# Performance work log

Hardware: AMD Instinct MI355X
Metric: run time of the kernel (lower is better)

The kernel has to match this reference:

```python
import jax, jax.numpy as jnp
import numpy as np

IOU_THR = 0.5
SCORE_THR = 0.5
MAX_OUT = 300  # max_output_boxes_per_batch


def setup_inputs() -> dict:
    key = jax.random.key(0)
    kb, ks = jax.random.split(key)
    B, N, C = 8, 1024, 32
    u = jax.random.uniform(kb, (B, N, 4), dtype=jnp.float32)
    ctr = u[..., :2] * 100.0          # box centers in [0,100)
    sz = u[..., 2:] * 20.0 + 1.0      # box sizes in [1,21)
    # y1x1y2x2 format (as the torch module expects)
    boxes = jnp.concatenate([ctr - 0.5 * sz, ctr + 0.5 * sz], axis=-1)
    scores = jax.random.uniform(ks, (B, N, C), dtype=jnp.float32)
    return {"boxes": boxes, "scores": scores}


def _pairwise_iou(b):
    # b: [C, N, 4] in y1x1y2x2; IoU is invariant to the axis swap so no
    # conversion to x1y1x2y2 is needed.
    y1, x1, y2, x2 = b[..., 0], b[..., 1], b[..., 2], b[..., 3]
    area = (y2 - y1) * (x2 - x1)                          # [C, N]
    yy1 = jnp.maximum(y1[..., :, None], y1[..., None, :])
    xx1 = jnp.maximum(x1[..., :, None], x1[..., None, :])
    yy2 = jnp.minimum(y2[..., :, None], y2[..., None, :])
    xx2 = jnp.minimum(x2[..., :, None], x2[..., None, :])
    inter = jnp.clip(yy2 - yy1, 0.0) * jnp.clip(xx2 - xx1, 0.0)
    return inter / (area[..., :, None] + area[..., None, :] - inter)


def _nms_keep(iou, valid, thr):
    # Sequential greedy suppression, vectorized across classes.
    # iou: [C, N, N] (score-descending order), valid: [C, N] bool.
    N = iou.shape[-1]
    idx = jnp.arange(N)

    def body(i, keep):
        sup = (iou[:, i, :] > thr) & keep[:, i][:, None] & (idx[None, :] > i)
        return keep & ~sup

    return jax.lax.fori_loop(0, N, body, valid)


def _nms_single(boxes, scores):
    # boxes: [N, 4], scores: [N, C]  ->  ([M,4], [M], [M])
    N, C = scores.shape
    M = MAX_OUT
    sc = scores.T                                  # [C, N]
    valid = sc > SCORE_THR
    s = jnp.where(valid, sc, -jnp.inf)
    order = jnp.argsort(-s, axis=1, stable=True)   # per-class score desc
    sb = boxes[order]                              # [C, N, 4]
    ss = jnp.take_along_axis(s, order, axis=1)     # [C, N]
    sv = jnp.take_along_axis(valid, order, axis=1)
    keep = _nms_keep(_pairwise_iou(sb), sv, IOU_THR)   # [C, N]

    # flatten class-major (matches torch scores.transpose(1,0).flatten())
    fb = sb.reshape(C * N, 4)
    fs = ss.reshape(-1)
    fk = keep.reshape(-1)
    fcls = jnp.repeat(jnp.arange(C, dtype=jnp.int32), N)
    fbind = order.reshape(-1)                      # original box index

    # global score-descending order over kept detections, truncate to M
    g = jnp.where(fk, fs, -jnp.inf)
    gord = jnp.argsort(-g, stable=True)[:M]
    tb, ts, tc, ti, tv = fb[gord], fs[gord], fcls[gord], fbind[gord], fk[gord]

    # dedup by original box index: keep highest-score (first) occurrence;
    # torch's _get_unique_first_indices re-orders by ascending box index.
    p = jnp.arange(M, dtype=jnp.int32)
    first = jnp.full((N,), M, dtype=jnp.int32).at[ti].min(jnp.where(tv, p, M))
    present = first < M                            # [N]
    ordN = jnp.argsort(~present, stable=True)[:M]  # present box ids, ascending
    pos = first[ordN]
    m = present[ordN]
    posc = jnp.where(m, pos, 0)
    out_boxes = jnp.where(m[:, None], tb[posc], 0.0)
    out_scores = jnp.where(m, ts[posc], 0.0)
    out_classes = jnp.where(m, tc[posc], 0)
    return out_boxes, out_scores, out_classes


def reference(boxes, scores):
    ob, osc, ocl = jax.vmap(_nms_single)(boxes, scores)
    # matches torch return (output_boxes, output_scores, output_classes)
    return ob, osc, ocl
```

## Files before the change

kernel.cpp:

```cpp
#include <hip/hip_runtime.h>

#pragma clang fp contract(off)

#define NBOX   1024
#define NCLS   32
#define NBATCH 8
#define MAXOUT 300
#define SMAX   11
#define MAGIC  0x600DF00Du

#define IOU_SUP(ab, aa, bj, arj, act, acc) do {               \
    float yy1 = fmaxf((ab).x, (bj).x);                        \
    float xx1 = fmaxf((ab).y, (bj).y);                        \
    float yy2 = fminf((ab).z, (bj).z);                        \
    float xx2 = fminf((ab).w, (bj).w);                        \
    float ih = fmaxf(yy2 - yy1, 0.0f);                        \
    float iw = fmaxf(xx2 - xx1, 0.0f);                        \
    float inter = ih * iw;                                    \
    float denom = ((aa) + (arj)) - inter;                     \
    float lhs = (inter + inter) - denom;                      \
    float rhs = denom * 5.9604644775390625e-08f;              \
    if ((act) && (lhs > rhs)) (acc) |= bit;                   \
  } while (0)

__device__ __forceinline__ unsigned long long shflx64(unsigned long long v, int m) {
  unsigned lo = (unsigned)__shfl_xor((int)(unsigned)v, m, 64);
  unsigned hi = (unsigned)__shfl_xor((int)(unsigned)(v >> 32), m, 64);
  return ((unsigned long long)hi << 32) | lo;
}

__device__ __forceinline__ unsigned long long cexch(
    unsigned long long mine, int jj, int kk, int t) {
  unsigned long long other = shflx64(mine, jj);
  bool iLow = ((t & jj) == 0);
  bool desc = ((t & kk) == 0);
  bool wantMax = (iLow == desc);
  bool otherBigger = (other > mine);
  return (wantMax == otherBigger) ? other : mine;
}

__global__ __launch_bounds__(1024) void nms_fused(
    const float* __restrict__ boxes, const float* __restrict__ scores,
    unsigned long long* __restrict__ recs, unsigned int* __restrict__ flags,
    float* __restrict__ out) {
#pragma clang fp contract(off)
  const int bc = blockIdx.x;
  const int b = bc & (NBATCH - 1);
  const int c = bc >> 3;
  const int t = threadIdx.x;
  const int lane = t & 63, wav = t >> 6;

  __shared__ __align__(16) unsigned char shraw[63488];
  unsigned long long* key = (unsigned long long*)shraw;
  float4* sbox            = (float4*)(shraw + 8192);
  float* sarea            = (float*)(shraw + 24576);
  unsigned long long* mask = (unsigned long long*)(shraw + 28672);
  __shared__ unsigned long long kb[16];
  __shared__ int shV;

  const float* sp = scores + (size_t)b * NBOX * NCLS + c;
  float s = sp[(size_t)t * NCLS];
  bool valid = (s > 0.5f);
  unsigned long long mine = valid
      ? ((((unsigned long long)__float_as_uint(s)) << 32) | (unsigned)(NBOX - 1 - t))
      : (unsigned long long)(unsigned)(NBOX - 1 - t);
  if (t == 0) shV = 0;
  if (t < 16) kb[t] = 0ull;
  __syncthreads();
  unsigned long long vb = __ballot(valid);
  if (lane == 0) atomicAdd(&shV, (int)__popcll(vb));

  for (int kk = 2; kk <= 64; kk <<= 1)
    for (int jj = kk >> 1; jj > 0; jj >>= 1)
      mine = cexch(mine, jj, kk, t);
  key[t] = mine;
  __syncthreads();
  for (int kk = 128; kk <= 1024; kk <<= 1) {
    for (int jj = kk >> 1; jj >= 64; jj >>= 1) {
      if (t < 512) {
        int i = ((t & ~(jj - 1)) << 1) | (t & (jj - 1));
        int ixj = i | jj;
        unsigned long long a = key[i], bb = key[ixj];
        if (((i & kk) == 0) ? (a < bb) : (a > bb)) { key[i] = bb; key[ixj] = a; }
      }
      __syncthreads();
    }
    mine = key[t];
    for (int jj = 32; jj > 0; jj >>= 1) mine = cexch(mine, jj, kk, t);
    key[t] = mine;
    __syncthreads();
  }

  int n0 = NBOX - 1 - (int)(mine & (NBOX - 1));
  const float4* gb = (const float4*)boxes + (size_t)b * NBOX;
  float4 bx4 = gb[n0];
  sbox[t] = bx4;
  sarea[t] = (bx4.z - bx4.x) * (bx4.w - bx4.y);
  __syncthreads();
  const int V = shV;
  const int S = (V + 63) >> 6;
  const bool aj = (t < V);

  unsigned long long mext[15];
  unsigned long long mself = 0ull;
#pragma unroll
  for (int w = 0; w < 15; ++w) mext[w] = 0ull;

  if (S <= SMAX) {
    int NC = 0;
    for (int I2 = 0; I2 < S; ++I2) NC += (S - I2 + 2) / 3;
    for (int k = wav; k < NC; k += 16) {
      int I = 0, rem = k;
      for (;;) { int cI = (S - I + 2) / 3; if (rem < cI) break; rem -= cI; ++I; }
      const int J0 = I + 3 * rem;
      const bool h1 = (J0 + 1 < S), h2 = (J0 + 2 < S);
      const int j0 = (J0 << 6) + lane;
      const int j1 = h1 ? j0 + 64 : j0;
      const int j2 = h2 ? j0 + 128 : j0;
      const float4 b0 = sbox[j0]; const float ar0 = sarea[j0];
      const float4 b1 = sbox[j1]; const float ar1 = sarea[j1];
      const float4 b2 = sbox[j2]; const float ar2 = sarea[j2];
      const bool act0 = (j0 < V);
      const bool act1 = h1 && (j0 + 64 < V);
      const bool act2 = h2 && (j0 + 128 < V);
      const float4* bi = &sbox[I << 6];
      const float* ai = &sarea[I << 6];
      unsigned long long a0 = 0, a1 = 0, a2 = 0;
      unsigned long long bit = 1ull;
#pragma unroll 8
      for (int q = 0; q < 64; ++q) {
        float4 ab = bi[q];
        float aa = ai[q];
        IOU_SUP(ab, aa, b0, ar0, act0, a0);
        IOU_SUP(ab, aa, b1, ar1, act1, a1);
        IOU_SUP(ab, aa, b2, ar2, act2, a2);
        bit <<= 1;
      }
      if (rem == 0) a0 &= (1ull << lane) - 1ull;
      const int vrem = V - (I << 6);
      if (vrem < 64) {
        unsigned long long tm = (1ull << vrem) - 1ull;
        a0 &= tm; a1 &= tm; a2 &= tm;
      }
      mask[(((J0 * (J0 + 1) / 2) << 6) + lane * (J0 + 1)) + I] = a0;
      if (h1) mask[((((J0 + 1) * (J0 + 2) / 2) << 6) + lane * (J0 + 2)) + I] = a1;
      if (h2) mask[((((J0 + 2) * (J0 + 3) / 2) << 6) + lane * (J0 + 3)) + I] = a2;
    }
    __syncthreads();
    if (t < (S << 6)) {
      const int J = wav;
      const int rbs = ((J * (J + 1) / 2) << 6) + lane * (J + 1);
#pragma unroll
      for (int I = 0; I < 15; ++I)
        if (I < J) mext[I] = mask[rbs + I];
      mself = mask[rbs + J];
    }
  } else {
    const int J = wav;
    const float4 bj = sbox[t];
    const float arj = sarea[t];
#pragma unroll
    for (int I = 0; I < 16; ++I) {
      if (I <= J && (I << 6) < V) {
        unsigned long long acc = 0, bit = 1ull;
        for (int q = 0; q < 64; ++q) {
          int i = (I << 6) + q;
          float4 ab = sbox[i];
          float aa = sarea[i];
          bool act = aj && (i < t) && (i < V);
          IOU_SUP(ab, aa, bj, arj, act, acc);
          bit <<= 1;
        }
        if (I == J) mself = acc;
        else mext[I] = acc;
      }
    }
  }
  __syncthreads();

  for (int w = 0; w < S; ++w) {
    if (wav == w) {
      bool supExt = false;
#pragma unroll
      for (int i = 0; i < 15; ++i)
        if (i < w) supExt = supExt || ((mext[i] & kb[i]) != 0ull);
      bool alive = aj && !supExt;
      unsigned long long cur = __ballot(alive);
      for (;;) {
        unsigned long long nb = __ballot(alive && ((mself & cur) == 0ull));
        if (nb == cur) break;
        cur = nb;
      }
      if (lane == 0) kb[w] = cur;
    }
    __syncthreads();
  }

  unsigned long long kbr[16];
#pragma unroll
  for (int w = 0; w < 16; ++w) kbr[w] = kb[w];
  int tot = 0;
#pragma unroll
  for (int w = 0; w < 16; ++w) tot += (int)__popcll(kbr[w]);
  const size_t rbase = ((size_t)b * NCLS + c) * MAXOUT;
  unsigned long long kw = kbr[0];
#pragma unroll
  for (int w = 1; w < 16; ++w) if (w == wav) kw = kbr[w];
  if (aj && ((kw >> lane) & 1ull)) {
    int rank = 0;
#pragma unroll
    for (int w = 0; w < 16; ++w)
      if (w < wav) rank += (int)__popcll(kbr[w]);
    rank += (int)__popcll(kw & ((1ull << lane) - 1ull));
    if (rank < MAXOUT) {
      unsigned sbits = (unsigned)(mine >> 32);
      int n = NBOX - 1 - (int)(mine & (NBOX - 1));
      int flat = c * NBOX + t;
      recs[rbase + rank] = (((unsigned long long)sbits) << 32)
          | ((unsigned)(NCLS * NBOX - 1 - flat) << 10) | (unsigned)n;
    }
  }
  if (t < MAXOUT && t >= tot) recs[rbase + t] = 0ull;

  __syncthreads();
  if (t == 0)
    __hip_atomic_store(&flags[bc], MAGIC, __ATOMIC_RELEASE,
                       __HIP_MEMORY_SCOPE_AGENT);
  if (c != 0) return;

  if (t < NCLS)
    while (__hip_atomic_load(&flags[(t << 3) + b], __ATOMIC_ACQUIRE,
                             __HIP_MEMORY_SCOPE_AGENT) != MAGIC)
      __builtin_amdgcn_s_sleep(8);
  __syncthreads();

  int* histw              = (int*)shraw;
  int* hist               = (int*)(shraw + 16384);
  int* suf                = (int*)(shraw + 17408);
  unsigned long long* maxKey = (unsigned long long*)(shraw + 18448);
  unsigned long long* blist  = (unsigned long long*)(shraw + 26640);
  __shared__ int bcnt;
  __shared__ unsigned long long shT;
  __shared__ int shBstar;
  __shared__ int wcnt[16], woff[16];
  __shared__ int shPresTot;

  const int CAND = NCLS * MAXOUT;
  unsigned long long* rb = recs + (size_t)b * NCLS * MAXOUT;
  unsigned long long cand[10];
#pragma unroll
  for (int q = 0; q < 10; ++q) {
    int j = t + (q << 10);
    cand[q] = (j < CAND)
        ? __hip_atomic_load(&rb[j], __ATOMIC_RELAXED, __HIP_MEMORY_SCOPE_AGENT)
        : 0ull;
  }
  maxKey[t] = 0;
#pragma unroll
  for (int q = 0; q < 4; ++q) histw[t + (q << 10)] = 0;
  if (t == 0) { bcnt = 0; shT = 0; shBstar = -1; }
  __syncthreads();

#pragma unroll
  for (int q = 0; q < 10; ++q) {
    unsigned long long v = cand[q];
    if (v != 0ull) {
      int bk = (int)(((unsigned)(v >> 32) - 0x3F000000u) >> 15);
      atomicAdd(&histw[(wav << 8) + bk], 1);
    }
  }
  __syncthreads();
  if (t < 256) {
    int ssum = 0;
#pragma unroll
    for (int w = 0; w < 16; ++w) ssum += histw[(w << 8) + t];
    hist[t] = ssum;
  }
  __syncthreads();

  if (wav == 0) {
    int h[4];
#pragma unroll
    for (int g = 0; g < 4; ++g) h[g] = hist[g * 64 + lane];
#pragma unroll
    for (int g = 0; g < 4; ++g) {
      int v = h[g];
#pragma unroll
      for (int off = 1; off < 64; off <<= 1) {
        int u = __shfl_down(v, off);
        if (lane + off < 64) v += u;
      }
      h[g] = v;
    }
    int sum1 = __shfl(h[1], 0);
    int sum2 = __shfl(h[2], 0);
    int sum3 = __shfl(h[3], 0);
    suf[0 * 64 + lane] = h[0] + sum1 + sum2 + sum3;
    suf[1 * 64 + lane] = h[1] + sum2 + sum3;
    suf[2 * 64 + lane] = h[2] + sum3;
    suf[3 * 64 + lane] = h[3];
    if (lane == 0) suf[256] = 0;
  }
  __syncthreads();

  if (t < 256) {
    if (suf[t] >= MAXOUT && suf[t + 1] < MAXOUT) shBstar = t;
  }
  __syncthreads();
  const int Bstar = shBstar;

  if (Bstar >= 0) {
#pragma unroll
    for (int q = 0; q < 10; ++q) {
      unsigned long long v = cand[q];
      if (v != 0ull) {
        int bk = (int)(((unsigned)(v >> 32) - 0x3F000000u) >> 15);
        if (bk == Bstar) { int idx = atomicAdd(&bcnt, 1); blist[idx] = v; }
      }
    }
    __syncthreads();
    int M = bcnt;
    int need = MAXOUT - suf[Bstar + 1];
    if (t < M) {
      unsigned long long mk = blist[t];
      int r = 0;
      for (int i = 0; i < M; ++i) r += (blist[i] > mk) ? 1 : 0;
      if (r == need - 1) shT = mk;
    }
    __syncthreads();
  }
  const unsigned long long T = shT;

#pragma unroll
  for (int q = 0; q < 10; ++q) {
    unsigned long long v = cand[q];
    if (v != 0ull && v >= T) {
      int n = (int)(v & (NBOX - 1));
      atomicMax(&maxKey[n], v);
    }
  }
  __syncthreads();

  bool pres = (maxKey[t] != 0ull);
  unsigned long long wm = __ballot(pres);
  if (lane == 0) wcnt[wav] = (int)__popcll(wm);
  __syncthreads();
  if (t < 16) {
    int v = wcnt[t];
    int inc = v;
#pragma unroll
    for (int off = 1; off < 16; off <<= 1) {
      int u = __shfl_up(inc, off);
      if (lane >= off) inc += u;
    }
    woff[t] = inc - v;
    if (t == 15) shPresTot = inc;
  }
  __syncthreads();
  const int total = shPresTot;

  float* ob = out + (size_t)b * MAXOUT * 4;
  float* os = out + (size_t)NBATCH * MAXOUT * 4 + (size_t)b * MAXOUT;
  float* oc = out + (size_t)NBATCH * MAXOUT * 5 + (size_t)b * MAXOUT;

  if (pres) {
    int slot = woff[wav] + (int)__popcll(wm & ((1ull << lane) - 1ull));
    unsigned long long v = maxKey[t];
    float score = __uint_as_float((unsigned)(v >> 32));
    int flat = NCLS * NBOX - 1 - (int)((v >> 10) & (unsigned)(NCLS * NBOX - 1));
    int cls = flat >> 10;
    float4 bx = ((const float4*)boxes)[(size_t)b * NBOX + t];
    ob[slot * 4 + 0] = bx.x;
    ob[slot * 4 + 1] = bx.y;
    ob[slot * 4 + 2] = bx.z;
    ob[slot * 4 + 3] = bx.w;
    os[slot] = score;
    oc[slot] = (float)cls;
  }
  if (t >= total && t < MAXOUT) {
    ob[t * 4 + 0] = 0.0f; ob[t * 4 + 1] = 0.0f;
    ob[t * 4 + 2] = 0.0f; ob[t * 4 + 3] = 0.0f;
    os[t] = 0.0f;
    oc[t] = 0.0f;
  }
}

extern "C" void kernel_launch(void* const* d_in, const int* in_sizes, int n_in,
                              void* d_out, int out_size, void* d_ws, size_t ws_size,
                              hipStream_t stream) {
  const float* boxes  = (const float*)d_in[0];
  const float* scores = (const float*)d_in[1];
  float* out = (float*)d_out;

  unsigned long long* recs = (unsigned long long*)d_ws;
  unsigned int* flags = (unsigned int*)((char*)d_ws +
      (size_t)NBATCH * NCLS * MAXOUT * sizeof(unsigned long long));

  nms_fused<<<NBATCH * NCLS, 1024, 0, stream>>>(boxes, scores, recs, flags, out);
}
```

Baseline: 102.6 us.

## Replace IoU mask matrix with sequential greedy NMS against kept list

The full 1024-key bitonic sort is replaced by bucketing valid scores into 16 score buckets of 64, each sorted with a wave-local bitonic sort and concatenated by prefix offsets. The full-sort path stays as a fallback when a bucket overflows. The triangular pairwise IoU bitmask and its ballot fixed-point resolution are replaced by a per-wave greedy pass. Each candidate is tested only against the boxes already kept, held in shared memory, and intra-wave suppression uses readlane broadcasts of the current leader. This avoids computing IoUs for suppressed pairs and shrinks shared memory, but the work becomes serial across waves and depends on how many boxes are kept.

```diff
diff --git a/kernel.cpp b/kernel.cpp
--- a/kernel.cpp
+++ b/kernel.cpp
@@ -6,22 +6,22 @@
 #define NCLS   32
 #define NBATCH 8
 #define MAXOUT 300
-#define SMAX   11
 #define MAGIC  0x600DF00Du
 
-#define IOU_SUP(ab, aa, bj, arj, act, acc) do {               \
-    float yy1 = fmaxf((ab).x, (bj).x);                        \
-    float xx1 = fmaxf((ab).y, (bj).y);                        \
-    float yy2 = fminf((ab).z, (bj).z);                        \
-    float xx2 = fminf((ab).w, (bj).w);                        \
-    float ih = fmaxf(yy2 - yy1, 0.0f);                        \
-    float iw = fmaxf(xx2 - xx1, 0.0f);                        \
-    float inter = ih * iw;                                    \
-    float denom = ((aa) + (arj)) - inter;                     \
-    float lhs = (inter + inter) - denom;                      \
-    float rhs = denom * 5.9604644775390625e-08f;              \
-    if ((act) && (lhs > rhs)) (acc) |= bit;                   \
-  } while (0)
+__device__ __forceinline__ bool sup_pred(float4 a, float aa, float4 bj, float arj) {
+#pragma clang fp contract(off)
+  float yy1 = fmaxf(a.x, bj.x);
+  float xx1 = fmaxf(a.y, bj.y);
+  float yy2 = fminf(a.z, bj.z);
+  float xx2 = fminf(a.w, bj.w);
+  float ih = fmaxf(yy2 - yy1, 0.0f);
+  float iw = fmaxf(xx2 - xx1, 0.0f);
+  float inter = ih * iw;
+  float denom = (aa + arj) - inter;
+  float lhs = (inter + inter) - denom;
+  float rhs = denom * 5.9604644775390625e-08f;
+  return lhs > rhs;
+}
 
 __device__ __forceinline__ unsigned long long shflx64(unsigned long long v, int m) {
   unsigned lo = (unsigned)__shfl_xor((int)(unsigned)v, m, 64);
@@ -37,6 +37,10 @@
   bool wantMax = (iLow == desc);
   bool otherBigger = (other > mine);
   return (wantMax == otherBigger) ? other : mine;
+}
+
+__device__ __forceinline__ float bcastf(float v, int p) {
+  return __uint_as_float((unsigned)__builtin_amdgcn_readlane((int)__float_as_uint(v), p));
 }
 
 __global__ __launch_bounds__(1024) void nms_fused(
@@ -50,13 +54,13 @@
   const int t = threadIdx.x;
   const int lane = t & 63, wav = t >> 6;
 
-  __shared__ __align__(16) unsigned char shraw[63488];
-  unsigned long long* key = (unsigned long long*)shraw;
-  float4* sbox            = (float4*)(shraw + 8192);
-  float* sarea            = (float*)(shraw + 24576);
-  unsigned long long* mask = (unsigned long long*)(shraw + 28672);
-  __shared__ unsigned long long kb[16];
-  __shared__ int shV;
+  __shared__ __align__(16) unsigned char shraw[36864];
+  unsigned long long* skey   = (unsigned long long*)shraw;
+  unsigned long long* bstage = (unsigned long long*)(shraw + 8192);
+  float4* kbox               = (float4*)(shraw + 16384);
+  float* karea               = (float*)(shraw + 32768);
+  __shared__ int bcount[16];
+  __shared__ int shOVF, shK;
 
   const float* sp = scores + (size_t)b * NBOX * NCLS + c;
   float s = sp[(size_t)t * NCLS];
@@ -64,162 +68,114 @@
   unsigned long long mine = valid
       ? ((((unsigned long long)__float_as_uint(s)) << 32) | (unsigned)(NBOX - 1 - t))
       : (unsigned long long)(unsigned)(NBOX - 1 - t);
-  if (t == 0) shV = 0;
-  if (t < 16) kb[t] = 0ull;
-  __syncthreads();
-  unsigned long long vb = __ballot(valid);
-  if (lane == 0) atomicAdd(&shV, (int)__popcll(vb));
-
-  for (int kk = 2; kk <= 64; kk <<= 1)
-    for (int jj = kk >> 1; jj > 0; jj >>= 1)
-      mine = cexch(mine, jj, kk, t);
-  key[t] = mine;
-  __syncthreads();
-  for (int kk = 128; kk <= 1024; kk <<= 1) {
-    for (int jj = kk >> 1; jj >= 64; jj >>= 1) {
-      if (t < 512) {
-        int i = ((t & ~(jj - 1)) << 1) | (t & (jj - 1));
-        int ixj = i | jj;
-        unsigned long long a = key[i], bb = key[ixj];
-        if (((i & kk) == 0) ? (a < bb) : (a > bb)) { key[i] = bb; key[ixj] = a; }
-      }
+  if (t < 16) bcount[t] = 0;
+  if (t == 0) { shOVF = 0; shK = 0; }
+  __syncthreads();
+
+  if (valid) {
+    int sbk = 15 - (int)((__float_as_uint(s) - 0x3F000000u) >> 19);
+    int slot = atomicAdd(&bcount[sbk], 1);
+    if (slot < 64) bstage[(sbk << 6) + slot] = mine;
+    else shOVF = 1;
+  }
+  __syncthreads();
+
+  int cval = (lane < 16) ? bcount[lane] : 0;
+  int incl = cval;
+#pragma unroll
+  for (int o = 1; o < 16; o <<= 1) {
+    int u = __shfl_up(incl, o);
+    if (lane >= o) incl += u;
+  }
+  const int V = __builtin_amdgcn_readlane(incl, 15);
+  const int myoff = __builtin_amdgcn_readlane(incl, wav) - bcount[wav];
+  const int mycnt = bcount[wav];
+
+  if (!shOVF) {
+    unsigned long long kreg = (lane < mycnt) ? bstage[(wav << 6) + lane] : 0ull;
+    for (int kk = 2; kk <= 64; kk <<= 1)
+      for (int jj = kk >> 1; jj > 0; jj >>= 1)
+        kreg = cexch(kreg, jj, kk, lane);
+    if (lane < mycnt) skey[myoff + lane] = kreg;
+    __syncthreads();
+  } else {
+    for (int kk = 2; kk <= 64; kk <<= 1)
+      for (int jj = kk >> 1; jj > 0; jj >>= 1)
+        mine = cexch(mine, jj, kk, t);
+    skey[t] = mine;
+    __syncthreads();
+    for (int kk = 128; kk <= 1024; kk <<= 1) {
+      for (int jj = kk >> 1; jj >= 64; jj >>= 1) {
+        if (t < 512) {
+          int i = ((t & ~(jj - 1)) << 1) | (t & (jj - 1));
+          int ixj = i | jj;
+          unsigned long long a = skey[i], bb = skey[ixj];
+          if (((i & kk) == 0) ? (a < bb) : (a > bb)) { skey[i] = bb; skey[ixj] = a; }
+        }
+        __syncthreads();
+      }
+      mine = skey[t];
+      for (int jj = 32; jj > 0; jj >>= 1) mine = cexch(mine, jj, kk, t);
+      skey[t] = mine;
       __syncthreads();
     }
-    mine = key[t];
-    for (int jj = 32; jj > 0; jj >>= 1) mine = cexch(mine, jj, kk, t);
-    key[t] = mine;
-    __syncthreads();
-  }
-
-  int n0 = NBOX - 1 - (int)(mine & (NBOX - 1));
+  }
+
   const float4* gb = (const float4*)boxes + (size_t)b * NBOX;
-  float4 bx4 = gb[n0];
-  sbox[t] = bx4;
-  sarea[t] = (bx4.z - bx4.x) * (bx4.w - bx4.y);
-  __syncthreads();
-  const int V = shV;
+  float4 mybox = make_float4(0.f, 0.f, 0.f, 0.f);
+  float myarea = 0.f;
+  unsigned long long mykey = 0ull;
+  if (t < V) {
+    mykey = skey[t];
+    int n0 = NBOX - 1 - (int)(mykey & (NBOX - 1));
+    mybox = gb[n0];
+    myarea = (mybox.z - mybox.x) * (mybox.w - mybox.y);
+  }
+  __syncthreads();
+
   const int S = (V + 63) >> 6;
-  const bool aj = (t < V);
-
-  unsigned long long mext[15];
-  unsigned long long mself = 0ull;
-#pragma unroll
-  for (int w = 0; w < 15; ++w) mext[w] = 0ull;
-
-  if (S <= SMAX) {
-    int NC = 0;
-    for (int I2 = 0; I2 < S; ++I2) NC += (S - I2 + 2) / 3;
-    for (int k = wav; k < NC; k += 16) {
-      int I = 0, rem = k;
-      for (;;) { int cI = (S - I + 2) / 3; if (rem < cI) break; rem -= cI; ++I; }
-      const int J0 = I + 3 * rem;
-      const bool h1 = (J0 + 1 < S), h2 = (J0 + 2 < S);
-      const int j0 = (J0 << 6) + lane;
-      const int j1 = h1 ? j0 + 64 : j0;
-      const int j2 = h2 ? j0 + 128 : j0;
-      const float4 b0 = sbox[j0]; const float ar0 = sarea[j0];
-      const float4 b1 = sbox[j1]; const float ar1 = sarea[j1];
-      const float4 b2 = sbox[j2]; const float ar2 = sarea[j2];
-      const bool act0 = (j0 < V);
-      const bool act1 = h1 && (j0 + 64 < V);
-      const bool act2 = h2 && (j0 + 128 < V);
-      const float4* bi = &sbox[I << 6];
-      const float* ai = &sarea[I << 6];
-      unsigned long long a0 = 0, a1 = 0, a2 = 0;
-      unsigned long long bit = 1ull;
-#pragma unroll 8
-      for (int q = 0; q < 64; ++q) {
-        float4 ab = bi[q];
-        float aa = ai[q];
-        IOU_SUP(ab, aa, b0, ar0, act0, a0);
-        IOU_SUP(ab, aa, b1, ar1, act1, a1);
-        IOU_SUP(ab, aa, b2, ar2, act2, a2);
-        bit <<= 1;
-      }
-      if (rem == 0) a0 &= (1ull << lane) - 1ull;
-      const int vrem = V - (I << 6);
-      if (vrem < 64) {
-        unsigned long long tm = (1ull << vrem) - 1ull;
-        a0 &= tm; a1 &= tm; a2 &= tm;
-      }
-      mask[(((J0 * (J0 + 1) / 2) << 6) + lane * (J0 + 1)) + I] = a0;
-      if (h1) mask[((((J0 + 1) * (J0 + 2) / 2) << 6) + lane * (J0 + 2)) + I] = a1;
-      if (h2) mask[((((J0 + 2) * (J0 + 3) / 2) << 6) + lane * (J0 + 3)) + I] = a2;
-    }
-    __syncthreads();
-    if (t < (S << 6)) {
-      const int J = wav;
-      const int rbs = ((J * (J + 1) / 2) << 6) + lane * (J + 1);
-#pragma unroll
-      for (int I = 0; I < 15; ++I)
-        if (I < J) mext[I] = mask[rbs + I];
-      mself = mask[rbs + J];
-    }
-  } else {
-    const int J = wav;
-    const float4 bj = sbox[t];
-    const float arj = sarea[t];
-#pragma unroll
-    for (int I = 0; I < 16; ++I) {
-      if (I <= J && (I << 6) < V) {
-        unsigned long long acc = 0, bit = 1ull;
-        for (int q = 0; q < 64; ++q) {
-          int i = (I << 6) + q;
-          float4 ab = sbox[i];
-          float aa = sarea[i];
-          bool act = aj && (i < t) && (i < V);
-          IOU_SUP(ab, aa, bj, arj, act, acc);
-          bit <<= 1;
-        }
-        if (I == J) mself = acc;
-        else mext[I] = acc;
-      }
-    }
-  }
-  __syncthreads();
-
-  for (int w = 0; w < S; ++w) {
-    if (wav == w) {
-      bool supExt = false;
-#pragma unroll
-      for (int i = 0; i < 15; ++i)
-        if (i < w) supExt = supExt || ((mext[i] & kb[i]) != 0ull);
-      bool alive = aj && !supExt;
-      unsigned long long cur = __ballot(alive);
-      for (;;) {
-        unsigned long long nb = __ballot(alive && ((mself & cur) == 0ull));
-        if (nb == cur) break;
-        cur = nb;
-      }
-      if (lane == 0) kb[w] = cur;
-    }
-    __syncthreads();
-  }
-
-  unsigned long long kbr[16];
-#pragma unroll
-  for (int w = 0; w < 16; ++w) kbr[w] = kb[w];
-  int tot = 0;
-#pragma unroll
-  for (int w = 0; w < 16; ++w) tot += (int)__popcll(kbr[w]);
+  bool kept = false;
+  int myrank = 0;
+  for (int ph = 0; ph < S; ++ph) {
+    if (wav == ph) {
+      int len = V - (ph << 6); if (len > 64) len = 64;
+      bool alive = (lane < len);
+      const int K = shK;
+      for (int k2 = 0; k2 < K; ++k2) {
+        float4 ab = kbox[k2];
+        float aa = karea[k2];
+        alive = alive && !sup_pred(ab, aa, mybox, myarea);
+      }
+      unsigned long long rem = __ballot(alive);
+      unsigned long long keptThis = 0ull;
+      while (rem) {
+        int p = (int)__builtin_ctzll(rem);
+        keptThis |= (1ull << p);
+        rem &= rem - 1ull;
+        if (!rem) break;
+        float4 pb = make_float4(bcastf(mybox.x, p), bcastf(mybox.y, p),
+                                bcastf(mybox.z, p), bcastf(mybox.w, p));
+        float pa = bcastf(myarea, p);
+        bool kill = ((rem >> lane) & 1ull) && sup_pred(pb, pa, mybox, myarea);
+        rem &= ~__ballot(kill);
+      }
+      kept = ((keptThis >> lane) & 1ull) != 0ull;
+      int idx = K + (int)__popcll(keptThis & ((1ull << lane) - 1ull));
+      if (kept) { kbox[idx] = mybox; karea[idx] = myarea; myrank = idx; }
+      if (lane == 0) shK = K + (int)__popcll(keptThis);
+    }
+    __syncthreads();
+  }
+
   const size_t rbase = ((size_t)b * NCLS + c) * MAXOUT;
-  unsigned long long kw = kbr[0];
-#pragma unroll
-  for (int w = 1; w < 16; ++w) if (w == wav) kw = kbr[w];
-  if (aj && ((kw >> lane) & 1ull)) {
-    int rank = 0;
-#pragma unroll
-    for (int w = 0; w < 16; ++w)
-      if (w < wav) rank += (int)__popcll(kbr[w]);
-    rank += (int)__popcll(kw & ((1ull << lane) - 1ull));
-    if (rank < MAXOUT) {
-      unsigned sbits = (unsigned)(mine >> 32);
-      int n = NBOX - 1 - (int)(mine & (NBOX - 1));
-      int flat = c * NBOX + t;
-      recs[rbase + rank] = (((unsigned long long)sbits) << 32)
-          | ((unsigned)(NCLS * NBOX - 1 - flat) << 10) | (unsigned)n;
-    }
-  }
+  if (kept && myrank < MAXOUT) {
+    unsigned sbits = (unsigned)(mykey >> 32);
+    int n = NBOX - 1 - (int)(mykey & (NBOX - 1));
+    int flat = c * NBOX + t;
+    recs[rbase + myrank] = (((unsigned long long)sbits) << 32)
+        | ((unsigned)(NCLS * NBOX - 1 - flat) << 10) | (unsigned)n;
+  }
+  int tot = shK; if (tot > MAXOUT) tot = MAXOUT;
   if (t < MAXOUT && t >= tot) recs[rbase + t] = 0ull;
 
   __syncthreads();
@@ -234,9 +190,9 @@
       __builtin_amdgcn_s_sleep(8);
   __syncthreads();
 
-  int* histw              = (int*)shraw;
-  int* hist               = (int*)(shraw + 16384);
-  int* suf                = (int*)(shraw + 17408);
+  int* histw                 = (int*)shraw;
+  int* hist                  = (int*)(shraw + 16384);
+  int* suf                   = (int*)(shraw + 17408);
   unsigned long long* maxKey = (unsigned long long*)(shraw + 18448);
   unsigned long long* blist  = (unsigned long long*)(shraw + 26640);
   __shared__ int bcnt;
@@ -246,13 +202,13 @@
   __shared__ int shPresTot;
 
   const int CAND = NCLS * MAXOUT;
-  unsigned long long* rb = recs + (size_t)b * NCLS * MAXOUT;
+  unsigned long long* rbp = recs + (size_t)b * NCLS * MAXOUT;
   unsigned long long cand[10];
 #pragma unroll
   for (int q = 0; q < 10; ++q) {
     int j = t + (q << 10);
     cand[q] = (j < CAND)
-        ? __hip_atomic_load(&rb[j], __ATOMIC_RELAXED, __HIP_MEMORY_SCOPE_AGENT)
+        ? __hip_atomic_load(&rbp[j], __ATOMIC_RELAXED, __HIP_MEMORY_SCOPE_AGENT)
         : 0ull;
   }
   maxKey[t] = 0;
```

Result: slower. 319.1 us (+211.0%).

## Replace full 1024-key bitonic sort with score-bucketed per-wave sorts

Applied to the files above, without the earlier changes.

Valid boxes are scattered into 16 score buckets in shared memory by their float exponent/mantissa bits. Each bucket is then sorted by a single wave using a 64-element register bitonic network, and buckets are placed with a prefix sum. This avoids the block-wide bitonic sort and its many __syncthreads barriers. If any bucket overflows 64 entries, the code falls back to the full sort, which costs an extra branch and shared staging.

```diff
diff --git a/kernel.cpp b/kernel.cpp
--- a/kernel.cpp
+++ b/kernel.cpp
@@ -51,12 +51,14 @@
   const int lane = t & 63, wav = t >> 6;
 
   __shared__ __align__(16) unsigned char shraw[63488];
-  unsigned long long* key = (unsigned long long*)shraw;
-  float4* sbox            = (float4*)(shraw + 8192);
-  float* sarea            = (float*)(shraw + 24576);
-  unsigned long long* mask = (unsigned long long*)(shraw + 28672);
+  unsigned long long* skey   = (unsigned long long*)shraw;
+  float4* sbox               = (float4*)(shraw + 8192);
+  float* sarea               = (float*)(shraw + 24576);
+  unsigned long long* mask   = (unsigned long long*)(shraw + 28672);
+  unsigned long long* bstage = (unsigned long long*)(shraw + 28672);
   __shared__ unsigned long long kb[16];
-  __shared__ int shV;
+  __shared__ int bcount[16];
+  __shared__ int shV, shOVF;
 
   const float* sp = scores + (size_t)b * NBOX * NCLS + c;
   float s = sp[(size_t)t * NCLS];
@@ -64,40 +66,68 @@
   unsigned long long mine = valid
       ? ((((unsigned long long)__float_as_uint(s)) << 32) | (unsigned)(NBOX - 1 - t))
       : (unsigned long long)(unsigned)(NBOX - 1 - t);
-  if (t == 0) shV = 0;
-  if (t < 16) kb[t] = 0ull;
+  if (t < 16) { bcount[t] = 0; kb[t] = 0ull; }
+  if (t == 0) { shV = 0; shOVF = 0; }
   __syncthreads();
   unsigned long long vb = __ballot(valid);
   if (lane == 0) atomicAdd(&shV, (int)__popcll(vb));
 
-  for (int kk = 2; kk <= 64; kk <<= 1)
-    for (int jj = kk >> 1; jj > 0; jj >>= 1)
-      mine = cexch(mine, jj, kk, t);
-  key[t] = mine;
-  __syncthreads();
-  for (int kk = 128; kk <= 1024; kk <<= 1) {
-    for (int jj = kk >> 1; jj >= 64; jj >>= 1) {
-      if (t < 512) {
-        int i = ((t & ~(jj - 1)) << 1) | (t & (jj - 1));
-        int ixj = i | jj;
-        unsigned long long a = key[i], bb = key[ixj];
-        if (((i & kk) == 0) ? (a < bb) : (a > bb)) { key[i] = bb; key[ixj] = a; }
-      }
+  if (valid) {
+    int sbk = 15 - (int)((__float_as_uint(s) - 0x3F000000u) >> 19);
+    int slot = atomicAdd(&bcount[sbk], 1);
+    if (slot < 64) bstage[(sbk << 6) + slot] = mine;
+    else shOVF = 1;
+  }
+  __syncthreads();
+  const int V = shV;
+
+  int cval = (lane < 16) ? bcount[lane] : 0;
+  int incl = cval;
+#pragma unroll
+  for (int o = 1; o < 16; o <<= 1) {
+    int u = __shfl_up(incl, o);
+    if (lane >= o) incl += u;
+  }
+  const int myoff = __builtin_amdgcn_readlane(incl, wav) - bcount[wav];
+  const int mycnt = bcount[wav];
+
+  if (!shOVF) {
+    unsigned long long kreg = (lane < mycnt) ? bstage[(wav << 6) + lane] : 0ull;
+    for (int kk = 2; kk <= 64; kk <<= 1)
+      for (int jj = kk >> 1; jj > 0; jj >>= 1)
+        kreg = cexch(kreg, jj, kk, lane);
+    if (lane < mycnt) skey[myoff + lane] = kreg;
+    __syncthreads();
+  } else {
+    for (int kk = 2; kk <= 64; kk <<= 1)
+      for (int jj = kk >> 1; jj > 0; jj >>= 1)
+        mine = cexch(mine, jj, kk, t);
+    skey[t] = mine;
+    __syncthreads();
+    for (int kk = 128; kk <= 1024; kk <<= 1) {
+      for (int jj = kk >> 1; jj >= 64; jj >>= 1) {
+        if (t < 512) {
+          int i = ((t & ~(jj - 1)) << 1) | (t & (jj - 1));
+          int ixj = i | jj;
+          unsigned long long a = skey[i], bb = skey[ixj];
+          if (((i & kk) == 0) ? (a < bb) : (a > bb)) { skey[i] = bb; skey[ixj] = a; }
+        }
+        __syncthreads();
+      }
+      mine = skey[t];
+      for (int jj = 32; jj > 0; jj >>= 1) mine = cexch(mine, jj, kk, t);
+      skey[t] = mine;
       __syncthreads();
     }
-    mine = key[t];
-    for (int jj = 32; jj > 0; jj >>= 1) mine = cexch(mine, jj, kk, t);
-    key[t] = mine;
-    __syncthreads();
-  }
-
-  int n0 = NBOX - 1 - (int)(mine & (NBOX - 1));
+  }
+
+  unsigned long long mykey = skey[t];
+  int n0 = NBOX - 1 - (int)(mykey & (NBOX - 1));
   const float4* gb = (const float4*)boxes + (size_t)b * NBOX;
   float4 bx4 = gb[n0];
   sbox[t] = bx4;
   sarea[t] = (bx4.z - bx4.x) * (bx4.w - bx4.y);
   __syncthreads();
-  const int V = shV;
   const int S = (V + 63) >> 6;
   const bool aj = (t < V);
 
@@ -213,14 +243,14 @@
       if (w < wav) rank += (int)__popcll(kbr[w]);
     rank += (int)__popcll(kw & ((1ull << lane) - 1ull));
     if (rank < MAXOUT) {
-      unsigned sbits = (unsigned)(mine >> 32);
-      int n = NBOX - 1 - (int)(mine & (NBOX - 1));
+      unsigned sbits = (unsigned)(mykey >> 32);
+      int n = NBOX - 1 - (int)(mykey & (NBOX - 1));
       int flat = c * NBOX + t;
       recs[rbase + rank] = (((unsigned long long)sbits) << 32)
           | ((unsigned)(NCLS * NBOX - 1 - flat) << 10) | (unsigned)n;
     }
   }
-  if (t < MAXOUT && t >= tot) recs[rbase + t] = 0ull;
+  if (t < MAXOUT && t >= ((tot < MAXOUT) ? tot : MAXOUT)) recs[rbase + t] = 0ull;
 
   __syncthreads();
   if (t == 0)
@@ -234,9 +264,9 @@
       __builtin_amdgcn_s_sleep(8);
   __syncthreads();
 
-  int* histw              = (int*)shraw;
-  int* hist               = (int*)(shraw + 16384);
-  int* suf                = (int*)(shraw + 17408);
+  int* histw                 = (int*)shraw;
+  int* hist                  = (int*)(shraw + 16384);
+  int* suf                   = (int*)(shraw + 17408);
   unsigned long long* maxKey = (unsigned long long*)(shraw + 18448);
   unsigned long long* blist  = (unsigned long long*)(shraw + 26640);
   __shared__ int bcnt;
@@ -246,13 +276,13 @@
   __shared__ int shPresTot;
 
   const int CAND = NCLS * MAXOUT;
-  unsigned long long* rb = recs + (size_t)b * NCLS * MAXOUT;
+  unsigned long long* rbp = recs + (size_t)b * NCLS * MAXOUT;
   unsigned long long cand[10];
 #pragma unroll
   for (int q = 0; q < 10; ++q) {
     int j = t + (q << 10);
     cand[q] = (j < CAND)
-        ? __hip_atomic_load(&rb[j], __ATOMIC_RELAXED, __HIP_MEMORY_SCOPE_AGENT)
+        ? __hip_atomic_load(&rbp[j], __ATOMIC_RELAXED, __HIP_MEMORY_SCOPE_AGENT)
         : 0ull;
   }
   maxKey[t] = 0;
```

Measured after the change: 99.01 us. 1.04x faster.
